# Performance work log

Hardware: AMD Instinct MI355X
Metric: run time of the kernel (lower is better)

The kernel has to match this reference:

```python
import jax, jax.numpy as jnp
import numpy as np

T, B, E = 2048, 2, 1024
H = 16
D = E // H


def setup_inputs() -> dict:
    key = jax.random.key(0)
    ks = jax.random.split(key, 7)
    s = 1.0 / np.sqrt(E)
    return {
        "query": jax.random.normal(ks[0], (T, B, E), jnp.float32),
        "key": jax.random.normal(ks[1], (T, B, E), jnp.float32),
        "value": jax.random.normal(ks[2], (T, B, E), jnp.float32),
        "in_proj_weight": jax.random.normal(ks[3], (3 * E, E), jnp.float32) * s,
        "in_proj_bias": jax.random.normal(ks[4], (3 * E,), jnp.float32) * 0.02,
        "out_proj_weight": jax.random.normal(ks[5], (E, E), jnp.float32) * s,
        "out_proj_bias": jax.random.normal(ks[6], (E,), jnp.float32) * 0.02,
    }


def reference(query, key, value, in_proj_weight, in_proj_bias, out_proj_weight, out_proj_bias):
    tgt_len, bsz, embed_dim = query.shape
    src_len = key.shape[0]
    head_dim = embed_dim // H
    # packed in-projection (F.linear: x @ W.T + b)
    w_q, w_k, w_v = jnp.split(in_proj_weight, 3, axis=0)
    b_q, b_k, b_v = jnp.split(in_proj_bias, 3, axis=0)
    q = query @ w_q.T + b_q   # [T, B, E]
    k = key @ w_k.T + b_k     # [S, B, E]
    v = value @ w_v.T + b_v   # [S, B, E]
    # [T,B,E] -> [B,H,T,D]
    q = q.reshape(tgt_len, bsz, H, head_dim).transpose(1, 2, 0, 3)
    k = k.reshape(src_len, bsz, H, head_dim).transpose(1, 2, 0, 3)
    v = v.reshape(src_len, bsz, H, head_dim).transpose(1, 2, 0, 3)
    scale = 1.0 / jnp.sqrt(jnp.asarray(head_dim, q.dtype))
    scores = jnp.einsum("bhtd,bhsd->bhts", q, k) * scale  # [B,H,T,S]
    attn_weights = jax.nn.softmax(scores, axis=-1)
    attn = jnp.einsum("bhts,bhsd->bhtd", attn_weights, v)  # [B,H,T,D]
    # [B,H,T,D] -> [T,B,E]
    attn = attn.transpose(2, 0, 1, 3).reshape(tgt_len, bsz, embed_dim)
    attn_output = attn @ out_proj_weight.T + out_proj_bias  # [T,B,E]
    # averaged attention weights over heads (average_attn_weights=True)
    avg_weights = jnp.sum(attn_weights, axis=1) / H  # [B,T,S]
    return attn_output, avg_weights
```

## Files before the change

kernel.cpp:

```cpp
#include <hip/hip_runtime.h>
#include <hip/hip_bf16.h>

typedef float  f32x2  __attribute__((ext_vector_type(2)));
typedef float  f32x4  __attribute__((ext_vector_type(4)));
typedef float  f32x16 __attribute__((ext_vector_type(16)));
typedef __bf16 bf16x8 __attribute__((ext_vector_type(8)));

#define MFMA16(A,B,C) __builtin_amdgcn_mfma_f32_16x16x32_bf16((A),(B),(C),0,0,0)
#define MFMA32(A,B,C) __builtin_amdgcn_mfma_f32_32x32x16_bf16((A),(B),(C),0,0,0)
#define EXP2(x) __builtin_amdgcn_exp2f(x)
#define LOG2(x) __builtin_amdgcn_logf(x)

static constexpr int Tn = 2048, Bn = 2, En = 1024, Hn = 16, Dn = 64;
static constexpr float kQScale = 0.125f * 1.4426950408889634f;

static __device__ __forceinline__ unsigned pack2(float a, float b) {
  union { __bf16 h[2]; unsigned u; } un;
  un.h[0] = (__bf16)a; un.h[1] = (__bf16)b;
  return un.u;
}

static __device__ __forceinline__ void gload_lds16(const void* g, void* l) {
  __builtin_amdgcn_global_load_lds(
      (const __attribute__((address_space(1))) void*)g,
      (__attribute__((address_space(3))) void*)l, 16, 0, 0);
}

__global__ __launch_bounds__(256)
void k_cvt(const float* __restrict__ q, const float* __restrict__ k,
           const float* __restrict__ v, const float* __restrict__ w3,
           const float* __restrict__ wo,
           __bf16* __restrict__ qb, __bf16* __restrict__ kb,
           __bf16* __restrict__ vb, __bf16* __restrict__ w3b,
           __bf16* __restrict__ wob)
{
  const size_t g = (size_t)blockIdx.x * 256 + threadIdx.x;
  const float* src;
  __bf16* dst;
  size_t off;
  if (g < 524288)        { src = q;  dst = qb;  off = g; }
  else if (g < 1048576)  { src = k;  dst = kb;  off = g - 524288; }
  else if (g < 1572864)  { src = v;  dst = vb;  off = g - 1048576; }
  else if (g < 1966080)  { src = w3; dst = w3b; off = g - 1572864; }
  else                   { src = wo; dst = wob; off = g - 1966080; }
  const float* p = src + off * 8;
  f32x4 a = *reinterpret_cast<const f32x4*>(p);
  f32x4 b = *reinterpret_cast<const f32x4*>(p + 4);
  bf16x8 o;
  #pragma unroll
  for (int e = 0; e < 4; ++e) { o[e] = (__bf16)a[e]; o[e + 4] = (__bf16)b[e]; }
  *reinterpret_cast<bf16x8*>(dst + off * 8) = o;
}

__global__ __launch_bounds__(256)
void k_qkv(const __bf16* __restrict__ Xq, const __bf16* __restrict__ Xk,
           const __bf16* __restrict__ Xv, const __bf16* __restrict__ W,
           const float* __restrict__ bias,
           __bf16* __restrict__ q_ws, __bf16* __restrict__ k_ws,
           __bf16* __restrict__ v_ws)
{
  __shared__ __align__(16) char a_lds[3][8192];
  __shared__ __align__(16) char b_lds[3][8192];
  const int tid = threadIdx.x;
  const int lane = tid & 63, w = tid >> 6;
  const int wr = w >> 1, wc = w & 1;
  const int ag = lane >> 4, lr = lane & 15;
  const int mBase = blockIdx.x * 128;
  const int oBase = blockIdx.y * 128;
  const int which = blockIdx.y >> 3;
  const __bf16* X  = (which == 0) ? Xq : ((which == 1) ? Xk : Xv);
  const __bf16* Wt = W + (size_t)oBase * En;
  __bf16* dst = (which == 0) ? q_ws : ((which == 1) ? k_ws : v_ws);
  const float oscale = (which == 0) ? kQScale : 1.0f;

  const int gA = w;
  const __bf16* pa0 = X  + (size_t)(mBase + lane) * En + gA * 8;
  const __bf16* pa1 = X  + (size_t)(mBase + 64 + lane) * En + gA * 8;
  const __bf16* pb0 = Wt + (size_t)(lane) * En + gA * 8;
  const __bf16* pb1 = Wt + (size_t)(64 + lane) * En + gA * 8;

#define STAGE(J, KK) do {                                                    \
    char* ab = a_lds[(J)];                                                   \
    char* bb = b_lds[(J)];                                                   \
    gload_lds16(pa0 + (KK), ab + gA * 2048);                                 \
    gload_lds16(pa1 + (KK), ab + gA * 2048 + 1024);                         \
    gload_lds16(pb0 + (KK), bb + gA * 2048);                                 \
    gload_lds16(pb1 + (KK), bb + gA * 2048 + 1024);                         \
  } while (0)

  f32x4 acc[4][4];
  #pragma unroll
  for (int i = 0; i < 4; ++i)
    #pragma unroll
    for (int j = 0; j < 4; ++j) { f32x4 z = {0.f, 0.f, 0.f, 0.f}; acc[i][j] = z; }

  STAGE(0, 0);
  STAGE(1, 32);

  for (int kt = 0; kt < 32; ++kt) {
    STAGE((kt + 2) % 3, ((kt + 2) & 31) * 32);
    asm volatile("s_waitcnt vmcnt(8)" ::: "memory");
    __builtin_amdgcn_s_barrier();
    __builtin_amdgcn_sched_barrier(0);
    const char* ac = a_lds[kt % 3];
    const char* bc = b_lds[kt % 3];
    bf16x8 af[4], bfr[4];
    #pragma unroll
    for (int mb = 0; mb < 4; ++mb)
      af[mb] = *(const bf16x8*)(ac + ag * 2048 + (wr * 64 + mb * 16 + lr) * 16);
    #pragma unroll
    for (int nb = 0; nb < 4; ++nb)
      bfr[nb] = *(const bf16x8*)(bc + ag * 2048 + (wc * 64 + nb * 16 + lr) * 16);
    #pragma unroll
    for (int mb = 0; mb < 4; ++mb)
      #pragma unroll
      for (int nb = 0; nb < 4; ++nb)
        acc[mb][nb] = MFMA16(af[mb], bfr[nb], acc[mb][nb]);
    asm volatile("s_waitcnt lgkmcnt(0)" ::: "memory");
    __builtin_amdgcn_sched_barrier(0);
    __builtin_amdgcn_s_barrier();
  }
#undef STAGE

  #pragma unroll
  for (int nb = 0; nb < 4; ++nb) {
    int oG = oBase + wc * 64 + nb * 16 + lr;
    float bv = bias[oG];
    int oS = oG & (En - 1);
    int h = oS >> 6, d = oS & 63;
    #pragma unroll
    for (int mb = 0; mb < 4; ++mb)
      #pragma unroll
      for (int r = 0; r < 4; ++r) {
        int i = mBase + wr * 64 + mb * 16 + ag * 4 + r;
        int t = i >> 1, b2 = i & 1;
        dst[(((size_t)(b2 * Hn + h)) * Tn + t) * Dn + d] =
            (__bf16)((acc[mb][nb][r] + bv) * oscale);
      }
  }
}

__global__ __launch_bounds__(256)
void k_transpose_v(const __bf16* __restrict__ v_ws, __bf16* __restrict__ vt_ws)
{
  __shared__ __bf16 tile[64][72];
  const int bh = blockIdx.x >> 5;
  const int tt = blockIdx.x & 31;
  const int tid = threadIdx.x;
  const __bf16* src = v_ws + ((size_t)bh * Tn + tt * 64) * Dn;
  #pragma unroll
  for (int it = 0; it < 2; ++it) {
    int gi = tid + it * 256;
    int row = gi >> 3, gg = gi & 7;
    *reinterpret_cast<bf16x8*>(&tile[row][gg * 8]) =
        *reinterpret_cast<const bf16x8*>(src + row * Dn + gg * 8);
  }
  __syncthreads();
  __bf16* dst = vt_ws + (size_t)bh * Dn * Tn + tt * 64;
  #pragma unroll
  for (int it = 0; it < 2; ++it) {
    int gi = tid + it * 256;
    int drow = gi >> 3, tg = gi & 7;
    bf16x8 vv;
    #pragma unroll
    for (int e = 0; e < 8; ++e) vv[e] = tile[tg * 8 + e][drow];
    *reinterpret_cast<bf16x8*>(dst + (size_t)drow * Tn + tg * 8) = vv;
  }
}

__global__ __launch_bounds__(256, 2)
void k_flash(const __bf16* __restrict__ q_ws, const __bf16* __restrict__ k_ws,
             const __bf16* __restrict__ vt_ws, __bf16* __restrict__ ctx,
             float* __restrict__ adj_g)
{
  __shared__ __align__(16) char kv_sm[2 * 16384];

  const int tid = threadIdx.x;
  const int lane = tid & 63, w = tid >> 6;
  const int tl = lane & 31, hi = lane >> 5;
  const int bh = blockIdx.x >> 4;
  const int qt = blockIdx.x & 15;
  const int t0w = qt * 128 + w * 32;

  const __bf16* kbase  = k_ws + (size_t)bh * Tn * Dn;
  const __bf16* vtbase = vt_ws + (size_t)bh * Dn * Tn;

  bf16x8 qf[4];
  {
    const __bf16* qrow = q_ws + ((size_t)bh * Tn + t0w + tl) * Dn + hi * 8;
    #pragma unroll
    for (int c = 0; c < 4; ++c)
      qf[c] = *reinterpret_cast<const bf16x8*>(qrow + c * 16);
  }

  union { unsigned u[4]; bf16x8 v; } onu;
  #pragma unroll
  for (int j = 0; j < 4; ++j) onu.u[j] = 0x3F803F80u;
  const bf16x8 kOne = onu.v;

  f32x16 accO0, accO1, accL;
  #pragma unroll
  for (int i = 0; i < 16; ++i) { accO0[i] = 0.f; accO1[i] = 0.f; accL[i] = 0.f; }
  float m_run = -INFINITY;

  const int r0 = tid >> 3, s0 = tid & 7;
  const int ldso = ((s0 ^ (r0 & 7)) << 4);
  const int ko0 = r0 * 128 + ldso;

  bf16x8 rk0 = *(const bf16x8*)(kbase + r0 * 64 + s0 * 8);
  bf16x8 rk1 = *(const bf16x8*)(kbase + (r0 + 32) * 64 + s0 * 8);
  bf16x8 rv0 = *(const bf16x8*)(vtbase + (size_t)r0 * Tn + s0 * 8);
  bf16x8 rv1 = *(const bf16x8*)(vtbase + (size_t)(r0 + 32) * Tn + s0 * 8);
  *(bf16x8*)(kv_sm + ko0) = rk0;
  *(bf16x8*)(kv_sm + ko0 + 4096) = rk1;
  *(bf16x8*)(kv_sm + 8192 + ko0) = rv0;
  *(bf16x8*)(kv_sm + 8192 + ko0 + 4096) = rv1;

  for (int st = 0; st < 32; ++st) {
    __syncthreads();
    const char* cur = kv_sm + (st & 1) * 16384;
    char* nxt = kv_sm + ((st + 1) & 1) * 16384;
    if (st + 1 < 32) {
      const __bf16* kn = kbase + (size_t)(st + 1) * 64 * Dn;
      const __bf16* vn = vtbase + (st + 1) * 64;
      rk0 = *(const bf16x8*)(kn + r0 * 64 + s0 * 8);
      rk1 = *(const bf16x8*)(kn + (r0 + 32) * 64 + s0 * 8);
      rv0 = *(const bf16x8*)(vn + (size_t)r0 * Tn + s0 * 8);
      rv1 = *(const bf16x8*)(vn + (size_t)(r0 + 32) * Tn + s0 * 8);
    }

    f32x16 sc0, sc1;
    #pragma unroll
    for (int i = 0; i < 16; ++i) { sc0[i] = 0.f; sc1[i] = 0.f; }
    const char* kr0 = cur + tl * 128;
    const char* kr1 = cur + (32 + tl) * 128;
    __builtin_amdgcn_s_setprio(1);
    #pragma unroll
    for (int c = 0; c < 4; ++c) {
      const int off = (((2 * c + hi) ^ (tl & 7)) << 4);
      sc0 = MFMA32(*(const bf16x8*)(kr0 + off), qf[c], sc0);
      sc1 = MFMA32(*(const bf16x8*)(kr1 + off), qf[c], sc1);
    }
    __builtin_amdgcn_s_setprio(0);

    float mx[8];
    #pragma unroll
    for (int i = 0; i < 8; ++i)
      mx[i] = fmaxf(fmaxf(sc0[i], sc0[i + 8]), fmaxf(sc1[i], sc1[i + 8]));
    float tm = fmaxf(fmaxf(fmaxf(mx[0], mx[1]), fmaxf(mx[2], mx[3])),
                     fmaxf(fmaxf(mx[4], mx[5]), fmaxf(mx[6], mx[7])));
    tm = fmaxf(tm, __shfl_xor(tm, 32, 64));
    if (__any(tm > m_run + 8.0f)) {
      const float mn = fmaxf(m_run, tm);
      const float es = EXP2(m_run - mn);
      m_run = mn;
      #pragma unroll
      for (int q = 0; q < 4; ++q)
        #pragma unroll
        for (int rr = 0; rr < 4; ++rr) {
          const float e = __shfl(es, 8 * q + 4 * hi + rr, 32);
          accO0[q * 4 + rr] *= e;
          accO1[q * 4 + rr] *= e;
          accL[q * 4 + rr] *= e;
        }
    }
    #pragma unroll
    for (int i = 0; i < 16; ++i) {
      sc0[i] = EXP2(sc0[i] - m_run);
      sc1[i] = EXP2(sc1[i] - m_run);
    }

    unsigned wA0[4], wB0[4], wA1[4], wB1[4];
    #pragma unroll
    for (int g = 0; g < 4; ++g) {
      wA0[g] = pack2(sc0[4 * g],     sc0[4 * g + 1]);
      wB0[g] = pack2(sc0[4 * g + 2], sc0[4 * g + 3]);
      wA1[g] = pack2(sc1[4 * g],     sc1[4 * g + 1]);
      wB1[g] = pack2(sc1[4 * g + 2], sc1[4 * g + 3]);
    }
    bf16x8 pa[2][2];
    #pragma unroll
    for (int sb = 0; sb < 2; ++sb) {
      const unsigned* WA = sb ? wA1 : wA0;
      const unsigned* WB = sb ? wB1 : wB0;
      #pragma unroll
      for (int c = 0; c < 2; ++c) {
        unsigned w0 = WA[2 * c], w2 = WA[2 * c + 1];
        unsigned w1 = WB[2 * c], w3 = WB[2 * c + 1];
        asm("v_permlane32_swap_b32 %0, %1" : "+v"(w0), "+v"(w2));
        asm("v_permlane32_swap_b32 %0, %1" : "+v"(w1), "+v"(w3));
        union { unsigned u[4]; bf16x8 v; } uu;
        uu.u[0] = w0; uu.u[1] = w1; uu.u[2] = w2; uu.u[3] = w3;
        pa[sb][c] = uu.v;
      }
    }

    const char* vr0 = cur + 8192 + tl * 128;
    const char* vr1 = cur + 8192 + (32 + tl) * 128;
    __builtin_amdgcn_s_setprio(1);
    #pragma unroll
    for (int sb = 0; sb < 2; ++sb)
      #pragma unroll
      for (int c = 0; c < 2; ++c) {
        const int off = (((sb * 4 + c * 2 + hi) ^ (tl & 7)) << 4);
        accO0 = MFMA32(pa[sb][c], *(const bf16x8*)(vr0 + off), accO0);
        accO1 = MFMA32(pa[sb][c], *(const bf16x8*)(vr1 + off), accO1);
        accL  = MFMA32(pa[sb][c], kOne, accL);
      }
    __builtin_amdgcn_s_setprio(0);

    if (st + 1 < 32) {
      *(bf16x8*)(nxt + ko0) = rk0;
      *(bf16x8*)(nxt + ko0 + 4096) = rk1;
      *(bf16x8*)(nxt + 8192 + ko0) = rv0;
      *(bf16x8*)(nxt + 8192 + ko0 + 4096) = rv1;
    }
  }

  const int b2 = bh >> 4, h = bh & 15;
  float adjv[16];
  #pragma unroll
  for (int q = 0; q < 4; ++q)
    #pragma unroll
    for (int rr = 0; rr < 4; ++rr) {
      const int j = q * 4 + rr;
      const float lv = 1.0f / accL[j];
      const int t = t0w + 8 * q + 4 * hi + rr;
      __bf16* cp = ctx + ((size_t)t * Bn + b2) * En + h * 64 + tl;
      cp[0]  = (__bf16)(accO0[j] * lv);
      cp[32] = (__bf16)(accO1[j] * lv);
      const float mrow = __shfl(m_run, 8 * q + 4 * hi + rr, 32);
      adjv[j] = mrow + LOG2(16.0f * accL[j]);
    }
  if (tl == 0) {
    #pragma unroll
    for (int q = 0; q < 4; ++q)
      #pragma unroll
      for (int rr = 0; rr < 4; ++rr) {
        const int t = t0w + 8 * q + 4 * hi + rr;
        adj_g[(size_t)bh * Tn + t] = adjv[q * 4 + rr];
      }
  }
}

__global__ __launch_bounds__(256)
void k_avgw(const __bf16* __restrict__ q_ws, const __bf16* __restrict__ k_ws,
            const float* __restrict__ adj_g, float* __restrict__ avg_out)
{
  __shared__ __align__(16) char q_sm[2][8192];
  __shared__ __align__(16) char k_sm[2][8192];
  __shared__ __align__(16) float adj_sm[16][64];

  const int tid = threadIdx.x;
  const int lane = tid & 63, w = tid >> 6;
  const int tl = lane & 31, hi = lane >> 5;
  const int b2 = blockIdx.x >> 10;
  const int tt = (blockIdx.x >> 5) & 31;
  const int ss = blockIdx.x & 31;
  const int thalf = (w >> 1) * 32, shalf = (w & 1) * 32;

  #pragma unroll
  for (int it = 0; it < 4; ++it) {
    int idx = tid + it * 256;
    int h = idx >> 6, trow = idx & 63;
    adj_sm[h][trow] = adj_g[((size_t)(b2 * Hn + h)) * Tn + tt * 64 + trow];
  }

  const size_t hstride = (size_t)Tn * Dn;
  const __bf16* qb = q_ws + ((size_t)(b2 * Hn) * Tn + tt * 64) * Dn;
  const __bf16* kb = k_ws + ((size_t)(b2 * Hn) * Tn + ss * 64) * Dn;

  const int r0 = tid >> 3, s0 = tid & 7;
  const int ldso = ((s0 ^ (r0 & 7)) << 4);
  const int ko0 = r0 * 128 + ldso;

  bf16x8 rq0 = *(const bf16x8*)(qb + r0 * 64 + s0 * 8);
  bf16x8 rq1 = *(const bf16x8*)(qb + (r0 + 32) * 64 + s0 * 8);
  bf16x8 rk0 = *(const bf16x8*)(kb + r0 * 64 + s0 * 8);
  bf16x8 rk1 = *(const bf16x8*)(kb + (r0 + 32) * 64 + s0 * 8);
  *(bf16x8*)(q_sm[0] + ko0) = rq0;
  *(bf16x8*)(q_sm[0] + ko0 + 4096) = rq1;
  *(bf16x8*)(k_sm[0] + ko0) = rk0;
  *(bf16x8*)(k_sm[0] + ko0 + 4096) = rk1;

  f32x16 avg;
  #pragma unroll
  for (int i = 0; i < 16; ++i) avg[i] = 0.f;

  for (int h = 0; h < Hn; ++h) {
    __syncthreads();
    const char* qc = q_sm[h & 1];
    const char* kc = k_sm[h & 1];
    char* qn = q_sm[(h + 1) & 1];
    char* kn = k_sm[(h + 1) & 1];
    if (h + 1 < Hn) {
      const __bf16* qp = qb + (size_t)(h + 1) * hstride;
      const __bf16* kp2 = kb + (size_t)(h + 1) * hstride;
      rq0 = *(const bf16x8*)(qp + r0 * 64 + s0 * 8);
      rq1 = *(const bf16x8*)(qp + (r0 + 32) * 64 + s0 * 8);
      rk0 = *(const bf16x8*)(kp2 + r0 * 64 + s0 * 8);
      rk1 = *(const bf16x8*)(kp2 + (r0 + 32) * 64 + s0 * 8);
    }

    f32x16 sc;
    #pragma unroll
    for (int i = 0; i < 16; ++i) sc[i] = 0.f;
    const char* qr = qc + (thalf + tl) * 128;
    const char* kr = kc + (shalf + tl) * 128;
    #pragma unroll
    for (int c = 0; c < 4; ++c) {
      const int off = (((2 * c + hi) ^ (tl & 7)) << 4);
      sc = MFMA32(*(const bf16x8*)(qr + off), *(const bf16x8*)(kr + off), sc);
    }

    #pragma unroll
    for (int q = 0; q < 4; ++q) {
      f32x4 ad = *(const f32x4*)&adj_sm[h][thalf + 8 * q + 4 * hi];
      #pragma unroll
      for (int r = 0; r < 4; ++r)
        avg[q * 4 + r] += EXP2(sc[q * 4 + r] - ad[r]);
    }

    if (h + 1 < Hn) {
      *(bf16x8*)(qn + ko0) = rq0;
      *(bf16x8*)(qn + ko0 + 4096) = rq1;
      *(bf16x8*)(kn + ko0) = rk0;
      *(bf16x8*)(kn + ko0 + 4096) = rk1;
    }
  }

  #pragma unroll
  for (int q = 0; q < 4; ++q)
    #pragma unroll
    for (int r = 0; r < 4; ++r) {
      int t = tt * 64 + thalf + 8 * q + 4 * hi + r;
      int s = ss * 64 + shalf + tl;
      avg_out[((size_t)(b2 * Tn + t)) * Tn + s] = avg[q * 4 + r];
    }
}

__global__ __launch_bounds__(256)
void k_outproj(const __bf16* __restrict__ ctx, const __bf16* __restrict__ W,
               const float* __restrict__ bias, float* __restrict__ out)
{
  __shared__ __align__(16) char a_lds[2][8192];
  __shared__ __align__(16) char b_lds[2][4096];
  const int tid = threadIdx.x;
  const int lane = tid & 63, w = tid >> 6;
  const int ag = lane >> 4, lr = lane & 15;
  const int mBase = blockIdx.x * 128;
  const int oBase = blockIdx.y * 64;

  const int srow = (w & 1) * 64 + lane;
  const int gw = w >> 1;
  const __bf16* paj[2];
  int aD[2];
  #pragma unroll
  for (int j = 0; j < 2; ++j) {
    const int g = 2 * j + gw;
    paj[j] = ctx + (size_t)(mBase + srow) * En + g * 8;
    aD[j] = g * 2048 + (w & 1) * 1024;
  }
  const __bf16* pb = W + (size_t)(oBase + lane) * En + w * 8;
  const int bDst = w * 1024;

  f32x4 acc[2][4];
  #pragma unroll
  for (int i = 0; i < 2; ++i)
    #pragma unroll
    for (int j = 0; j < 4; ++j) { f32x4 z = {0.f,0.f,0.f,0.f}; acc[i][j] = z; }

  #pragma unroll
  for (int j = 0; j < 2; ++j) gload_lds16(paj[j], &a_lds[0][aD[j]]);
  gload_lds16(pb, &b_lds[0][bDst]);
  __syncthreads();

  for (int kt = 0; kt < 32; ++kt) {
    const int cur = kt & 1, nxt = cur ^ 1;
    if (kt + 1 < 32) {
      const int kk = (kt + 1) * 32;
      #pragma unroll
      for (int j = 0; j < 2; ++j) gload_lds16(paj[j] + kk, &a_lds[nxt][aD[j]]);
      gload_lds16(pb + kk, &b_lds[nxt][bDst]);
    }
    bf16x8 af[2], bfr[4];
    #pragma unroll
    for (int mb = 0; mb < 2; ++mb)
      af[mb] = *(const bf16x8*)(&a_lds[cur][ag * 2048 + (w * 32 + mb * 16 + lr) * 16]);
    #pragma unroll
    for (int nb = 0; nb < 4; ++nb)
      bfr[nb] = *(const bf16x8*)(&b_lds[cur][ag * 1024 + (nb * 16 + lr) * 16]);
    #pragma unroll
    for (int mb = 0; mb < 2; ++mb)
      #pragma unroll
      for (int nb = 0; nb < 4; ++nb)
        acc[mb][nb] = MFMA16(af[mb], bfr[nb], acc[mb][nb]);
    __syncthreads();
  }

  #pragma unroll
  for (int nb = 0; nb < 4; ++nb) {
    int o = oBase + nb * 16 + lr;
    float bv = bias[o];
    #pragma unroll
    for (int mb = 0; mb < 2; ++mb)
      #pragma unroll
      for (int r = 0; r < 4; ++r) {
        int i = mBase + w * 32 + mb * 16 + ag * 4 + r;
        out[(size_t)i * En + o] = acc[mb][nb][r] + bv;
      }
  }
}

extern "C" void kernel_launch(void* const* d_in, const int* in_sizes, int n_in,
                              void* d_out, int out_size, void* d_ws, size_t ws_size,
                              hipStream_t stream)
{
  (void)in_sizes; (void)n_in; (void)out_size; (void)ws_size;
  const float* query = (const float*)d_in[0];
  const float* key   = (const float*)d_in[1];
  const float* value = (const float*)d_in[2];
  const float* in_w  = (const float*)d_in[3];
  const float* in_b  = (const float*)d_in[4];
  const float* out_w = (const float*)d_in[5];
  const float* out_b = (const float*)d_in[6];

  float* attn_out = (float*)d_out;
  float* avg_out  = (float*)d_out + (size_t)Tn * Bn * En;

  char* ws = (char*)d_ws;
  const size_t MB = 1u << 20;
  __bf16* q_ws  = (__bf16*)(ws);
  __bf16* k_ws  = (__bf16*)(ws + 8 * MB);
  __bf16* v_ws  = (__bf16*)(ws + 16 * MB);
  __bf16* vt_ws = (__bf16*)(ws + 24 * MB);
  __bf16* ctx   = (__bf16*)(ws + 32 * MB);
  float*  adj_g = (float*)(ws + 40 * MB);
  __bf16* xq_bf = vt_ws;
  __bf16* xk_bf = ctx;
  __bf16* xv_bf = (__bf16*)(ws + 40 * MB + 512 * 1024);
  __bf16* w3_bf = (__bf16*)(ws + 48 * MB + 512 * 1024);
  __bf16* wo_bf = (__bf16*)(ws + 54 * MB + 512 * 1024);

  k_cvt<<<8192, 256, 0, stream>>>(query, key, value, in_w, out_w,
                                  xq_bf, xk_bf, xv_bf, w3_bf, wo_bf);
  k_qkv<<<dim3(32, 24), 256, 0, stream>>>(xq_bf, xk_bf, xv_bf, w3_bf, in_b,
                                          q_ws, k_ws, v_ws);
  k_transpose_v<<<1024, 256, 0, stream>>>(v_ws, vt_ws);
  k_flash<<<512, 256, 0, stream>>>(q_ws, k_ws, vt_ws, ctx, adj_g);
  k_avgw<<<2048, 256, 0, stream>>>(q_ws, k_ws, adj_g, avg_out);
  k_outproj<<<dim3(32, 16), 256, 0, stream>>>(ctx, wo_bf, out_b, attn_out);
}
```

Measured before the change: 212.1 us.

## Halve block sizes for QKV GEMM and flash attention, doubling grid size

The QKV projection kernel now uses 128-thread blocks with a 128x64 output tile and a two-stage LDS double buffer, replacing the three-stage async pipeline with explicit waitcnt. This doubles the grid. The flash kernel moves to 128 threads, each block covering 64 query rows instead of 128, with 1024 blocks. The K/V staging loop is reworked so fewer threads each load four rows. The aim is more blocks to fill the CUs and better occupancy. The cost is more redundant K/V and weight traffic per output and a shallower load pipeline in the GEMM.

```diff
diff --git a/kernel.cpp b/kernel.cpp
--- a/kernel.cpp
+++ b/kernel.cpp
@@ -52,79 +52,82 @@
   *reinterpret_cast<bf16x8*>(dst + off * 8) = o;
 }
 
-__global__ __launch_bounds__(256)
+__global__ __launch_bounds__(128)
 void k_qkv(const __bf16* __restrict__ Xq, const __bf16* __restrict__ Xk,
            const __bf16* __restrict__ Xv, const __bf16* __restrict__ W,
            const float* __restrict__ bias,
            __bf16* __restrict__ q_ws, __bf16* __restrict__ k_ws,
            __bf16* __restrict__ v_ws)
 {
-  __shared__ __align__(16) char a_lds[3][8192];
-  __shared__ __align__(16) char b_lds[3][8192];
+  __shared__ __align__(16) char a_lds[2][8192];
+  __shared__ __align__(16) char b_lds[2][4096];
   const int tid = threadIdx.x;
   const int lane = tid & 63, w = tid >> 6;
-  const int wr = w >> 1, wc = w & 1;
   const int ag = lane >> 4, lr = lane & 15;
   const int mBase = blockIdx.x * 128;
-  const int oBase = blockIdx.y * 128;
-  const int which = blockIdx.y >> 3;
+  const int by = blockIdx.y;
+  const int which = by >> 4;
   const __bf16* X  = (which == 0) ? Xq : ((which == 1) ? Xk : Xv);
-  const __bf16* Wt = W + (size_t)oBase * En;
+  const __bf16* Wt = W + (size_t)by * 64 * En;
   __bf16* dst = (which == 0) ? q_ws : ((which == 1) ? k_ws : v_ws);
   const float oscale = (which == 0) ? kQScale : 1.0f;
 
-  const int gA = w;
-  const __bf16* pa0 = X  + (size_t)(mBase + lane) * En + gA * 8;
-  const __bf16* pa1 = X  + (size_t)(mBase + 64 + lane) * En + gA * 8;
-  const __bf16* pb0 = Wt + (size_t)(lane) * En + gA * 8;
-  const __bf16* pb1 = Wt + (size_t)(64 + lane) * En + gA * 8;
-
-#define STAGE(J, KK) do {                                                    \
-    char* ab = a_lds[(J)];                                                   \
-    char* bb = b_lds[(J)];                                                   \
-    gload_lds16(pa0 + (KK), ab + gA * 2048);                                 \
-    gload_lds16(pa1 + (KK), ab + gA * 2048 + 1024);                         \
-    gload_lds16(pb0 + (KK), bb + gA * 2048);                                 \
-    gload_lds16(pb1 + (KK), bb + gA * 2048 + 1024);                         \
+  const __bf16* paj[2][2];
+  const __bf16* pbj[2];
+  int aD[2][2], bD[2];
+  #pragma unroll
+  for (int j = 0; j < 2; ++j) {
+    const int g = 2 * w + j;
+    #pragma unroll
+    for (int h = 0; h < 2; ++h) {
+      paj[j][h] = X + (size_t)(mBase + h * 64 + lane) * En + g * 8;
+      aD[j][h] = g * 2048 + h * 1024;
+    }
+    pbj[j] = Wt + (size_t)lane * En + g * 8;
+    bD[j] = g * 1024;
+  }
+
+  f32x4 acc[4][4];
+  #pragma unroll
+  for (int i = 0; i < 4; ++i)
+    #pragma unroll
+    for (int j = 0; j < 4; ++j) { f32x4 z = {0.f, 0.f, 0.f, 0.f}; acc[i][j] = z; }
+
+#define STAGE(BUF, KK) do {                                                  \
+    _Pragma("unroll")                                                        \
+    for (int j = 0; j < 2; ++j) {                                            \
+      _Pragma("unroll")                                                      \
+      for (int h = 0; h < 2; ++h)                                            \
+        gload_lds16(paj[j][h] + (KK), &a_lds[BUF][aD[j][h]]);                \
+      gload_lds16(pbj[j] + (KK), &b_lds[BUF][bD[j]]);                        \
+    }                                                                        \
   } while (0)
 
-  f32x4 acc[4][4];
-  #pragma unroll
-  for (int i = 0; i < 4; ++i)
-    #pragma unroll
-    for (int j = 0; j < 4; ++j) { f32x4 z = {0.f, 0.f, 0.f, 0.f}; acc[i][j] = z; }
-
   STAGE(0, 0);
-  STAGE(1, 32);
+  __syncthreads();
 
   for (int kt = 0; kt < 32; ++kt) {
-    STAGE((kt + 2) % 3, ((kt + 2) & 31) * 32);
-    asm volatile("s_waitcnt vmcnt(8)" ::: "memory");
-    __builtin_amdgcn_s_barrier();
-    __builtin_amdgcn_sched_barrier(0);
-    const char* ac = a_lds[kt % 3];
-    const char* bc = b_lds[kt % 3];
+    const int cur = kt & 1, nxt = cur ^ 1;
+    if (kt + 1 < 32) STAGE(nxt, (kt + 1) * 32);
     bf16x8 af[4], bfr[4];
     #pragma unroll
     for (int mb = 0; mb < 4; ++mb)
-      af[mb] = *(const bf16x8*)(ac + ag * 2048 + (wr * 64 + mb * 16 + lr) * 16);
+      af[mb] = *(const bf16x8*)(&a_lds[cur][ag * 2048 + (w * 64 + mb * 16 + lr) * 16]);
     #pragma unroll
     for (int nb = 0; nb < 4; ++nb)
-      bfr[nb] = *(const bf16x8*)(bc + ag * 2048 + (wc * 64 + nb * 16 + lr) * 16);
+      bfr[nb] = *(const bf16x8*)(&b_lds[cur][ag * 1024 + (nb * 16 + lr) * 16]);
     #pragma unroll
     for (int mb = 0; mb < 4; ++mb)
       #pragma unroll
       for (int nb = 0; nb < 4; ++nb)
         acc[mb][nb] = MFMA16(af[mb], bfr[nb], acc[mb][nb]);
-    asm volatile("s_waitcnt lgkmcnt(0)" ::: "memory");
-    __builtin_amdgcn_sched_barrier(0);
-    __builtin_amdgcn_s_barrier();
+    __syncthreads();
   }
 #undef STAGE
 
   #pragma unroll
   for (int nb = 0; nb < 4; ++nb) {
-    int oG = oBase + wc * 64 + nb * 16 + lr;
+    int oG = by * 64 + nb * 16 + lr;
     float bv = bias[oG];
     int oS = oG & (En - 1);
     int h = oS >> 6, d = oS & 63;
@@ -132,7 +135,7 @@
     for (int mb = 0; mb < 4; ++mb)
       #pragma unroll
       for (int r = 0; r < 4; ++r) {
-        int i = mBase + wr * 64 + mb * 16 + ag * 4 + r;
+        int i = mBase + w * 64 + mb * 16 + ag * 4 + r;
         int t = i >> 1, b2 = i & 1;
         dst[(((size_t)(b2 * Hn + h)) * Tn + t) * Dn + d] =
             (__bf16)((acc[mb][nb][r] + bv) * oscale);
@@ -168,7 +171,7 @@
   }
 }
 
-__global__ __launch_bounds__(256, 2)
+__global__ __launch_bounds__(128, 2)
 void k_flash(const __bf16* __restrict__ q_ws, const __bf16* __restrict__ k_ws,
              const __bf16* __restrict__ vt_ws, __bf16* __restrict__ ctx,
              float* __restrict__ adj_g)
@@ -178,9 +181,9 @@
   const int tid = threadIdx.x;
   const int lane = tid & 63, w = tid >> 6;
   const int tl = lane & 31, hi = lane >> 5;
-  const int bh = blockIdx.x >> 4;
-  const int qt = blockIdx.x & 15;
-  const int t0w = qt * 128 + w * 32;
+  const int bh = blockIdx.x >> 5;
+  const int qt = blockIdx.x & 31;
+  const int t0w = qt * 64 + w * 32;
 
   const __bf16* kbase  = k_ws + (size_t)bh * Tn * Dn;
   const __bf16* vtbase = vt_ws + (size_t)bh * Dn * Tn;
@@ -207,14 +210,17 @@
   const int ldso = ((s0 ^ (r0 & 7)) << 4);
   const int ko0 = r0 * 128 + ldso;
 
-  bf16x8 rk0 = *(const bf16x8*)(kbase + r0 * 64 + s0 * 8);
-  bf16x8 rk1 = *(const bf16x8*)(kbase + (r0 + 32) * 64 + s0 * 8);
-  bf16x8 rv0 = *(const bf16x8*)(vtbase + (size_t)r0 * Tn + s0 * 8);
-  bf16x8 rv1 = *(const bf16x8*)(vtbase + (size_t)(r0 + 32) * Tn + s0 * 8);
-  *(bf16x8*)(kv_sm + ko0) = rk0;
-  *(bf16x8*)(kv_sm + ko0 + 4096) = rk1;
-  *(bf16x8*)(kv_sm + 8192 + ko0) = rv0;
-  *(bf16x8*)(kv_sm + 8192 + ko0 + 4096) = rv1;
+  bf16x8 rk[4], rv[4];
+  #pragma unroll
+  for (int j = 0; j < 4; ++j) {
+    rk[j] = *(const bf16x8*)(kbase + (r0 + 16 * j) * 64 + s0 * 8);
+    rv[j] = *(const bf16x8*)(vtbase + (size_t)(r0 + 16 * j) * Tn + s0 * 8);
+  }
+  #pragma unroll
+  for (int j = 0; j < 4; ++j) {
+    *(bf16x8*)(kv_sm + ko0 + j * 2048) = rk[j];
+    *(bf16x8*)(kv_sm + 8192 + ko0 + j * 2048) = rv[j];
+  }
 
   for (int st = 0; st < 32; ++st) {
     __syncthreads();
@@ -223,10 +229,11 @@
     if (st + 1 < 32) {
       const __bf16* kn = kbase + (size_t)(st + 1) * 64 * Dn;
       const __bf16* vn = vtbase + (st + 1) * 64;
-      rk0 = *(const bf16x8*)(kn + r0 * 64 + s0 * 8);
-      rk1 = *(const bf16x8*)(kn + (r0 + 32) * 64 + s0 * 8);
-      rv0 = *(const bf16x8*)(vn + (size_t)r0 * Tn + s0 * 8);
-      rv1 = *(const bf16x8*)(vn + (size_t)(r0 + 32) * Tn + s0 * 8);
+      #pragma unroll
+      for (int j = 0; j < 4; ++j) {
+        rk[j] = *(const bf16x8*)(kn + (r0 + 16 * j) * 64 + s0 * 8);
+        rv[j] = *(const bf16x8*)(vn + (size_t)(r0 + 16 * j) * Tn + s0 * 8);
+      }
     }
 
     f32x16 sc0, sc1;
@@ -310,10 +317,11 @@
     __builtin_amdgcn_s_setprio(0);
 
     if (st + 1 < 32) {
-      *(bf16x8*)(nxt + ko0) = rk0;
-      *(bf16x8*)(nxt + ko0 + 4096) = rk1;
-      *(bf16x8*)(nxt + 8192 + ko0) = rv0;
-      *(bf16x8*)(nxt + 8192 + ko0 + 4096) = rv1;
+      #pragma unroll
+      for (int j = 0; j < 4; ++j) {
+        *(bf16x8*)(nxt + ko0 + j * 2048) = rk[j];
+        *(bf16x8*)(nxt + 8192 + ko0 + j * 2048) = rv[j];
+      }
     }
   }
 
@@ -544,10 +552,10 @@
 
   k_cvt<<<8192, 256, 0, stream>>>(query, key, value, in_w, out_w,
                                   xq_bf, xk_bf, xv_bf, w3_bf, wo_bf);
-  k_qkv<<<dim3(32, 24), 256, 0, stream>>>(xq_bf, xk_bf, xv_bf, w3_bf, in_b,
+  k_qkv<<<dim3(32, 48), 128, 0, stream>>>(xq_bf, xk_bf, xv_bf, w3_bf, in_b,
                                           q_ws, k_ws, v_ws);
   k_transpose_v<<<1024, 256, 0, stream>>>(v_ws, vt_ws);
-  k_flash<<<512, 256, 0, stream>>>(q_ws, k_ws, vt_ws, ctx, adj_g);
+  k_flash<<<1024, 128, 0, stream>>>(q_ws, k_ws, vt_ws, ctx, adj_g);
   k_avgw<<<2048, 256, 0, stream>>>(q_ws, k_ws, adj_g, avg_out);
   k_outproj<<<dim3(32, 16), 256, 0, stream>>>(ctx, wo_bf, out_b, attn_out);
 }
```

Result: slower. 245.0 us (+15.5%).

## Use register-prefetch triple-buffered LDS pipelines in QKV projection and flash kernels

Applied to the files above, without the earlier changes.

The QKV projection GEMM no longer uses direct global-to-LDS loads with explicit vmcnt waits. It now loads into registers, writes to one of three LDS buffers, and unrolls the loop by two with two register sets. The flash attention kernel's K/V staging moves from double to triple buffering with two register sets, so the prefetch distance is two tiles and only one barrier is needed per tile. The aim is to hide more global-load latency, at the cost of extra registers and more LDS per block, which can lower occupancy.

```diff
diff --git a/kernel.cpp b/kernel.cpp
--- a/kernel.cpp
+++ b/kernel.cpp
@@ -18,12 +18,6 @@
   union { __bf16 h[2]; unsigned u; } un;
   un.h[0] = (__bf16)a; un.h[1] = (__bf16)b;
   return un.u;
-}
-
-static __device__ __forceinline__ void gload_lds16(const void* g, void* l) {
-  __builtin_amdgcn_global_load_lds(
-      (const __attribute__((address_space(1))) void*)g,
-      (__attribute__((address_space(3))) void*)l, 16, 0, 0);
 }
 
 __global__ __launch_bounds__(256)
@@ -78,15 +72,40 @@
   const __bf16* pa1 = X  + (size_t)(mBase + 64 + lane) * En + gA * 8;
   const __bf16* pb0 = Wt + (size_t)(lane) * En + gA * 8;
   const __bf16* pb1 = Wt + (size_t)(64 + lane) * En + gA * 8;
-
-#define STAGE(J, KK) do {                                                    \
-    char* ab = a_lds[(J)];                                                   \
-    char* bb = b_lds[(J)];                                                   \
-    gload_lds16(pa0 + (KK), ab + gA * 2048);                                 \
-    gload_lds16(pa1 + (KK), ab + gA * 2048 + 1024);                         \
-    gload_lds16(pb0 + (KK), bb + gA * 2048);                                 \
-    gload_lds16(pb1 + (KK), bb + gA * 2048 + 1024);                         \
+  const int dA0 = gA * 2048 + lane * 16;
+  const int dA1 = gA * 2048 + 1024 + lane * 16;
+
+  bf16x8 aA0, aA1, bA0, bA1;
+  bf16x8 aB0, aB1, bB0, bB1;
+
+#define QLOAD(R0, R1, S0, S1, KK) do {                                       \
+    R0 = *(const bf16x8*)(pa0 + (KK));                                       \
+    R1 = *(const bf16x8*)(pa1 + (KK));                                       \
+    S0 = *(const bf16x8*)(pb0 + (KK));                                       \
+    S1 = *(const bf16x8*)(pb1 + (KK));                                       \
   } while (0)
+#define QWRITE(BUF, R0, R1, S0, S1) do {                                     \
+    *(bf16x8*)(&a_lds[(BUF)][dA0]) = R0;                                     \
+    *(bf16x8*)(&a_lds[(BUF)][dA1]) = R1;                                     \
+    *(bf16x8*)(&b_lds[(BUF)][dA0]) = S0;                                     \
+    *(bf16x8*)(&b_lds[(BUF)][dA1]) = S1;                                     \
+  } while (0)
+#define QCOMP(BUF) do {                                                      \
+    const char* ac = a_lds[(BUF)];                                           \
+    const char* bc = b_lds[(BUF)];                                           \
+    bf16x8 af[4], bfr[4];                                                    \
+    _Pragma("unroll")                                                        \
+    for (int mb = 0; mb < 4; ++mb)                                           \
+      af[mb] = *(const bf16x8*)(ac + ag * 2048 + (wr * 64 + mb * 16 + lr) * 16); \
+    _Pragma("unroll")                                                        \
+    for (int nb = 0; nb < 4; ++nb)                                           \
+      bfr[nb] = *(const bf16x8*)(bc + ag * 2048 + (wc * 64 + nb * 16 + lr) * 16); \
+    _Pragma("unroll")                                                        \
+    for (int mb = 0; mb < 4; ++mb)                                           \
+      _Pragma("unroll")                                                      \
+      for (int nb = 0; nb < 4; ++nb)                                         \
+        acc[mb][nb] = MFMA16(af[mb], bfr[nb], acc[mb][nb]);                  \
+  } while (0)
 
   f32x4 acc[4][4];
   #pragma unroll
@@ -94,33 +113,27 @@
     #pragma unroll
     for (int j = 0; j < 4; ++j) { f32x4 z = {0.f, 0.f, 0.f, 0.f}; acc[i][j] = z; }
 
-  STAGE(0, 0);
-  STAGE(1, 32);
-
-  for (int kt = 0; kt < 32; ++kt) {
-    STAGE((kt + 2) % 3, ((kt + 2) & 31) * 32);
-    asm volatile("s_waitcnt vmcnt(8)" ::: "memory");
-    __builtin_amdgcn_s_barrier();
-    __builtin_amdgcn_sched_barrier(0);
-    const char* ac = a_lds[kt % 3];
-    const char* bc = b_lds[kt % 3];
-    bf16x8 af[4], bfr[4];
-    #pragma unroll
-    for (int mb = 0; mb < 4; ++mb)
-      af[mb] = *(const bf16x8*)(ac + ag * 2048 + (wr * 64 + mb * 16 + lr) * 16);
-    #pragma unroll
-    for (int nb = 0; nb < 4; ++nb)
-      bfr[nb] = *(const bf16x8*)(bc + ag * 2048 + (wc * 64 + nb * 16 + lr) * 16);
-    #pragma unroll
-    for (int mb = 0; mb < 4; ++mb)
-      #pragma unroll
-      for (int nb = 0; nb < 4; ++nb)
-        acc[mb][nb] = MFMA16(af[mb], bfr[nb], acc[mb][nb]);
-    asm volatile("s_waitcnt lgkmcnt(0)" ::: "memory");
-    __builtin_amdgcn_sched_barrier(0);
-    __builtin_amdgcn_s_barrier();
-  }
-#undef STAGE
+  QLOAD(aA0, aA1, bA0, bA1, 0);
+  QWRITE(0, aA0, aA1, bA0, bA1);
+  QLOAD(aB0, aB1, bB0, bB1, 32);
+
+  int cb = 0;
+  for (int kt = 0; kt < 32; kt += 2) {
+    const int wb1 = (cb + 1 == 3) ? 0 : cb + 1;
+    const int wb2 = (wb1 + 1 == 3) ? 0 : wb1 + 1;
+    __syncthreads();
+    if (kt + 2 < 32) QLOAD(aA0, aA1, bA0, bA1, (kt + 2) * 32);
+    QCOMP(cb);
+    QWRITE(wb1, aB0, aB1, bB0, bB1);
+    __syncthreads();
+    if (kt + 3 < 32) QLOAD(aB0, aB1, bB0, bB1, (kt + 3) * 32);
+    QCOMP(wb1);
+    if (kt + 2 < 32) QWRITE(wb2, aA0, aA1, bA0, bA1);
+    cb = wb2;
+  }
+#undef QLOAD
+#undef QWRITE
+#undef QCOMP
 
   #pragma unroll
   for (int nb = 0; nb < 4; ++nb) {
@@ -173,7 +186,7 @@
              const __bf16* __restrict__ vt_ws, __bf16* __restrict__ ctx,
              float* __restrict__ adj_g)
 {
-  __shared__ __align__(16) char kv_sm[2 * 16384];
+  __shared__ __align__(16) char kv_sm[3 * 16384];
 
   const int tid = threadIdx.x;
   const int lane = tid & 63, w = tid >> 6;
@@ -207,115 +220,125 @@
   const int ldso = ((s0 ^ (r0 & 7)) << 4);
   const int ko0 = r0 * 128 + ldso;
 
-  bf16x8 rk0 = *(const bf16x8*)(kbase + r0 * 64 + s0 * 8);
-  bf16x8 rk1 = *(const bf16x8*)(kbase + (r0 + 32) * 64 + s0 * 8);
-  bf16x8 rv0 = *(const bf16x8*)(vtbase + (size_t)r0 * Tn + s0 * 8);
-  bf16x8 rv1 = *(const bf16x8*)(vtbase + (size_t)(r0 + 32) * Tn + s0 * 8);
-  *(bf16x8*)(kv_sm + ko0) = rk0;
-  *(bf16x8*)(kv_sm + ko0 + 4096) = rk1;
-  *(bf16x8*)(kv_sm + 8192 + ko0) = rv0;
-  *(bf16x8*)(kv_sm + 8192 + ko0 + 4096) = rv1;
-
-  for (int st = 0; st < 32; ++st) {
+  bf16x8 kA0, kA1, vA0, vA1;
+  bf16x8 kB0, kB1, vB0, vB1;
+
+#define FLOAD(K0, K1, V0, V1, ST) do {                                       \
+    const __bf16* kn = kbase + (size_t)(ST) * 64 * Dn;                       \
+    const __bf16* vn = vtbase + (ST) * 64;                                   \
+    K0 = *(const bf16x8*)(kn + r0 * 64 + s0 * 8);                            \
+    K1 = *(const bf16x8*)(kn + (r0 + 32) * 64 + s0 * 8);                     \
+    V0 = *(const bf16x8*)(vn + (size_t)r0 * Tn + s0 * 8);                    \
+    V1 = *(const bf16x8*)(vn + (size_t)(r0 + 32) * Tn + s0 * 8);             \
+  } while (0)
+#define FWRITE(BUF, K0, K1, V0, V1) do {                                     \
+    char* wb = kv_sm + (BUF) * 16384;                                        \
+    *(bf16x8*)(wb + ko0) = K0;                                               \
+    *(bf16x8*)(wb + ko0 + 4096) = K1;                                        \
+    *(bf16x8*)(wb + 8192 + ko0) = V0;                                        \
+    *(bf16x8*)(wb + 8192 + ko0 + 4096) = V1;                                 \
+  } while (0)
+#define FCOMP(BUF) do {                                                      \
+    const char* cur = kv_sm + (BUF) * 16384;                                 \
+    f32x16 sc0, sc1;                                                         \
+    _Pragma("unroll")                                                        \
+    for (int i = 0; i < 16; ++i) { sc0[i] = 0.f; sc1[i] = 0.f; }             \
+    const char* kr0 = cur + tl * 128;                                        \
+    const char* kr1 = cur + (32 + tl) * 128;                                 \
+    __builtin_amdgcn_s_setprio(1);                                           \
+    _Pragma("unroll")                                                        \
+    for (int c = 0; c < 4; ++c) {                                            \
+      const int off = (((2 * c + hi) ^ (tl & 7)) << 4);                      \
+      sc0 = MFMA32(*(const bf16x8*)(kr0 + off), qf[c], sc0);                 \
+      sc1 = MFMA32(*(const bf16x8*)(kr1 + off), qf[c], sc1);                 \
+    }                                                                        \
+    __builtin_amdgcn_s_setprio(0);                                           \
+    float mx[8];                                                             \
+    _Pragma("unroll")                                                        \
+    for (int i = 0; i < 8; ++i)                                              \
+      mx[i] = fmaxf(fmaxf(sc0[i], sc0[i + 8]), fmaxf(sc1[i], sc1[i + 8]));   \
+    float tm = fmaxf(fmaxf(fmaxf(mx[0], mx[1]), fmaxf(mx[2], mx[3])),        \
+                     fmaxf(fmaxf(mx[4], mx[5]), fmaxf(mx[6], mx[7])));       \
+    tm = fmaxf(tm, __shfl_xor(tm, 32, 64));                                  \
+    if (__any(tm > m_run + 8.0f)) {                                          \
+      const float mn = fmaxf(m_run, tm);                                     \
+      const float es = EXP2(m_run - mn);                                     \
+      m_run = mn;                                                            \
+      _Pragma("unroll")                                                      \
+      for (int q = 0; q < 4; ++q)                                            \
+        _Pragma("unroll")                                                    \
+        for (int rr = 0; rr < 4; ++rr) {                                     \
+          const float e = __shfl(es, 8 * q + 4 * hi + rr, 32);               \
+          accO0[q * 4 + rr] *= e;                                            \
+          accO1[q * 4 + rr] *= e;                                            \
+          accL[q * 4 + rr] *= e;                                             \
+        }                                                                    \
+    }                                                                        \
+    _Pragma("unroll")                                                        \
+    for (int i = 0; i < 16; ++i) {                                           \
+      sc0[i] = EXP2(sc0[i] - m_run);                                         \
+      sc1[i] = EXP2(sc1[i] - m_run);                                         \
+    }                                                                        \
+    unsigned wA0[4], wB0[4], wA1[4], wB1[4];                                 \
+    _Pragma("unroll")                                                        \
+    for (int g = 0; g < 4; ++g) {                                            \
+      wA0[g] = pack2(sc0[4 * g],     sc0[4 * g + 1]);                        \
+      wB0[g] = pack2(sc0[4 * g + 2], sc0[4 * g + 3]);                        \
+      wA1[g] = pack2(sc1[4 * g],     sc1[4 * g + 1]);                        \
+      wB1[g] = pack2(sc1[4 * g + 2], sc1[4 * g + 3]);                        \
+    }                                                                        \
+    bf16x8 pa[2][2];                                                         \
+    _Pragma("unroll")                                                        \
+    for (int sb = 0; sb < 2; ++sb) {                                         \
+      const unsigned* WA = sb ? wA1 : wA0;                                   \
+      const unsigned* WB = sb ? wB1 : wB0;                                   \
+      _Pragma("unroll")                                                      \
+      for (int c = 0; c < 2; ++c) {                                          \
+        unsigned w0 = WA[2 * c], w2 = WA[2 * c + 1];                         \
+        unsigned w1 = WB[2 * c], w3 = WB[2 * c + 1];                         \
+        asm("v_permlane32_swap_b32 %0, %1" : "+v"(w0), "+v"(w2));            \
+        asm("v_permlane32_swap_b32 %0, %1" : "+v"(w1), "+v"(w3));            \
+        union { unsigned u[4]; bf16x8 v; } uu;                               \
+        uu.u[0] = w0; uu.u[1] = w1; uu.u[2] = w2; uu.u[3] = w3;              \
+        pa[sb][c] = uu.v;                                                    \
+      }                                                                      \
+    }                                                                        \
+    const char* vr0 = cur + 8192 + tl * 128;                                 \
+    const char* vr1 = cur + 8192 + (32 + tl) * 128;                          \
+    __builtin_amdgcn_s_setprio(1);                                           \
+    _Pragma("unroll")                                                        \
+    for (int sb = 0; sb < 2; ++sb)                                           \
+      _Pragma("unroll")                                                      \
+      for (int c = 0; c < 2; ++c) {                                          \
+        const int off = (((sb * 4 + c * 2 + hi) ^ (tl & 7)) << 4);           \
+        accO0 = MFMA32(pa[sb][c], *(const bf16x8*)(vr0 + off), accO0);       \
+        accO1 = MFMA32(pa[sb][c], *(const bf16x8*)(vr1 + off), accO1);       \
+        accL  = MFMA32(pa[sb][c], kOne, accL);                               \
+      }                                                                      \
+    __builtin_amdgcn_s_setprio(0);                                           \
+  } while (0)
+
+  FLOAD(kA0, kA1, vA0, vA1, 0);
+  FWRITE(0, kA0, kA1, vA0, vA1);
+  FLOAD(kB0, kB1, vB0, vB1, 1);
+
+  int cb = 0;
+  for (int st = 0; st < 32; st += 2) {
+    const int wb1 = (cb + 1 == 3) ? 0 : cb + 1;
+    const int wb2 = (wb1 + 1 == 3) ? 0 : wb1 + 1;
     __syncthreads();
-    const char* cur = kv_sm + (st & 1) * 16384;
-    char* nxt = kv_sm + ((st + 1) & 1) * 16384;
-    if (st + 1 < 32) {
-      const __bf16* kn = kbase + (size_t)(st + 1) * 64 * Dn;
-      const __bf16* vn = vtbase + (st + 1) * 64;
-      rk0 = *(const bf16x8*)(kn + r0 * 64 + s0 * 8);
-      rk1 = *(const bf16x8*)(kn + (r0 + 32) * 64 + s0 * 8);
-      rv0 = *(const bf16x8*)(vn + (size_t)r0 * Tn + s0 * 8);
-      rv1 = *(const bf16x8*)(vn + (size_t)(r0 + 32) * Tn + s0 * 8);
-    }
-
-    f32x16 sc0, sc1;
-    #pragma unroll
-    for (int i = 0; i < 16; ++i) { sc0[i] = 0.f; sc1[i] = 0.f; }
-    const char* kr0 = cur + tl * 128;
-    const char* kr1 = cur + (32 + tl) * 128;
-    __builtin_amdgcn_s_setprio(1);
-    #pragma unroll
-    for (int c = 0; c < 4; ++c) {
-      const int off = (((2 * c + hi) ^ (tl & 7)) << 4);
-      sc0 = MFMA32(*(const bf16x8*)(kr0 + off), qf[c], sc0);
-      sc1 = MFMA32(*(const bf16x8*)(kr1 + off), qf[c], sc1);
-    }
-    __builtin_amdgcn_s_setprio(0);
-
-    float mx[8];
-    #pragma unroll
-    for (int i = 0; i < 8; ++i)
-      mx[i] = fmaxf(fmaxf(sc0[i], sc0[i + 8]), fmaxf(sc1[i], sc1[i + 8]));
-    float tm = fmaxf(fmaxf(fmaxf(mx[0], mx[1]), fmaxf(mx[2], mx[3])),
-                     fmaxf(fmaxf(mx[4], mx[5]), fmaxf(mx[6], mx[7])));
-    tm = fmaxf(tm, __shfl_xor(tm, 32, 64));
-    if (__any(tm > m_run + 8.0f)) {
-      const float mn = fmaxf(m_run, tm);
-      const float es = EXP2(m_run - mn);
-      m_run = mn;
-      #pragma unroll
-      for (int q = 0; q < 4; ++q)
-        #pragma unroll
-        for (int rr = 0; rr < 4; ++rr) {
-          const float e = __shfl(es, 8 * q + 4 * hi + rr, 32);
-          accO0[q * 4 + rr] *= e;
-          accO1[q * 4 + rr] *= e;
-          accL[q * 4 + rr] *= e;
-        }
-    }
-    #pragma unroll
-    for (int i = 0; i < 16; ++i) {
-      sc0[i] = EXP2(sc0[i] - m_run);
-      sc1[i] = EXP2(sc1[i] - m_run);
-    }
-
-    unsigned wA0[4], wB0[4], wA1[4], wB1[4];
-    #pragma unroll
-    for (int g = 0; g < 4; ++g) {
-      wA0[g] = pack2(sc0[4 * g],     sc0[4 * g + 1]);
-      wB0[g] = pack2(sc0[4 * g + 2], sc0[4 * g + 3]);
-      wA1[g] = pack2(sc1[4 * g],     sc1[4 * g + 1]);
-      wB1[g] = pack2(sc1[4 * g + 2], sc1[4 * g + 3]);
-    }
-    bf16x8 pa[2][2];
-    #pragma unroll
-    for (int sb = 0; sb < 2; ++sb) {
-      const unsigned* WA = sb ? wA1 : wA0;
-      const unsigned* WB = sb ? wB1 : wB0;
-      #pragma unroll
-      for (int c = 0; c < 2; ++c) {
-        unsigned w0 = WA[2 * c], w2 = WA[2 * c + 1];
-        unsigned w1 = WB[2 * c], w3 = WB[2 * c + 1];
-        asm("v_permlane32_swap_b32 %0, %1" : "+v"(w0), "+v"(w2));
-        asm("v_permlane32_swap_b32 %0, %1" : "+v"(w1), "+v"(w3));
-        union { unsigned u[4]; bf16x8 v; } uu;
-        uu.u[0] = w0; uu.u[1] = w1; uu.u[2] = w2; uu.u[3] = w3;
-        pa[sb][c] = uu.v;
-      }
-    }
-
-    const char* vr0 = cur + 8192 + tl * 128;
-    const char* vr1 = cur + 8192 + (32 + tl) * 128;
-    __builtin_amdgcn_s_setprio(1);
-    #pragma unroll
-    for (int sb = 0; sb < 2; ++sb)
-      #pragma unroll
-      for (int c = 0; c < 2; ++c) {
-        const int off = (((sb * 4 + c * 2 + hi) ^ (tl & 7)) << 4);
-        accO0 = MFMA32(pa[sb][c], *(const bf16x8*)(vr0 + off), accO0);
-        accO1 = MFMA32(pa[sb][c], *(const bf16x8*)(vr1 + off), accO1);
-        accL  = MFMA32(pa[sb][c], kOne, accL);
-      }
-    __builtin_amdgcn_s_setprio(0);
-
-    if (st + 1 < 32) {
-      *(bf16x8*)(nxt + ko0) = rk0;
-      *(bf16x8*)(nxt + ko0 + 4096) = rk1;
-      *(bf16x8*)(nxt + 8192 + ko0) = rv0;
-      *(bf16x8*)(nxt + 8192 + ko0 + 4096) = rv1;
-    }
-  }
+    if (st + 2 < 32) FLOAD(kA0, kA1, vA0, vA1, st + 2);
+    FCOMP(cb);
+    FWRITE(wb1, kB0, kB1, vB0, vB1);
+    __syncthreads();
+    if (st + 3 < 32) FLOAD(kB0, kB1, vB0, vB1, st + 3);
+    FCOMP(wb1);
+    if (st + 2 < 32) FWRITE(wb2, kA0, kA1, vA0, vA1);
+    cb = wb2;
+  }
+#undef FLOAD
+#undef FWRITE
+#undef FCOMP
 
   const int b2 = bh >> 4, h = bh & 15;
   float adjv[16];
@@ -439,6 +462,12 @@
     }
 }
 
+static __device__ __forceinline__ void gload_lds16(const void* g, void* l) {
+  __builtin_amdgcn_global_load_lds(
+      (const __attribute__((address_space(1))) void*)g,
+      (__attribute__((address_space(3))) void*)l, 16, 0, 0);
+}
+
 __global__ __launch_bounds__(256)
 void k_outproj(const __bf16* __restrict__ ctx, const __bf16* __restrict__ W,
                const float* __restrict__ bias, float* __restrict__ out)
```

New measurement: 212.5 us. No clear change (+0.2%).
